# Kernel optimization log

Hardware: AMD Instinct MI355X
Metric: run time of the kernel (lower is better)

The kernel has to match this reference:

```python
import jax, jax.numpy as jnp
import numpy as np

B, S, IN_DIM, LATENT, SYM = 16, 256, 512, 512, 128
NUM_NODES, NUM_CODES, MAX_OPS, MAX_BUS = 4, 512, 4, 32
HALT_EPS, MAX_SEQ = 1e-3, 256


def setup_inputs() -> dict:
    key = jax.random.key(0)
    ks = jax.random.split(key, 10)

    def lin(k, out_d, in_d, pre=()):
        kw, kb = jax.random.split(k)
        lim = 1.0 / np.sqrt(in_d).astype(np.float32)
        w = jax.random.uniform(kw, pre + (out_d, in_d), minval=-lim, maxval=lim, dtype=jnp.float32)
        b = jax.random.uniform(kb, pre + (out_d,), minval=-lim, maxval=lim, dtype=jnp.float32)
        return w, b

    x = jax.random.normal(ks[0], (B, S, IN_DIM), jnp.float32)
    ipw, ipb = lin(ks[1], LATENT, IN_DIM)
    tp = jax.random.normal(ks[2], (1, MAX_SEQ, LATENT), jnp.float32)
    N = (NUM_NODES,)
    sw, sb = lin(ks[3], SYM, LATENT, N)
    qw, qb = lin(ks[4], 1, SYM, N)
    rw, rb = lin(ks[5], LATENT, 2 * LATENT, N)
    c1w, c1b = lin(ks[6], LATENT, LATENT + SYM, N)
    c2w, c2b = lin(ks[7], LATENT, LATENT, N)
    cb = jax.random.normal(ks[8], (NUM_NODES, NUM_CODES, SYM), jnp.float32)
    return {"x": x, "input_proj_w": ipw, "input_proj_b": ipb, "token_prompts": tp,
            "sym_w": sw, "sym_b": sb, "qry_w": qw, "qry_b": qb,
            "read_w": rw, "read_b": rb, "c1_w": c1w, "c1_b": c1b,
            "c2_w": c2w, "c2_b": c2b, "codebook": cb}


def _forward(x, input_proj_w, input_proj_b, token_prompts, sym_w, sym_b, qry_w, qry_b,
             read_w, read_b, c1_w, c1_b, c2_w, c2_b, codebook):
    Bx, Sx, _ = x.shape
    N = Bx * Sx
    # input projection + positional prompts
    out = jnp.einsum('bsi,li->bsl', x, input_proj_w) + input_proj_b + token_prompts[:, :Sx, :]
    prev_out = out
    active = jnp.ones((Bx, Sx), bool)
    token_tags = jnp.zeros((Bx, Sx, SYM), x.dtype)
    # TensorBus rolling buffers ([max_bus, B, S, dim]); with default cfg the roll branch never fires
    sym_buf = jnp.zeros((MAX_BUS, Bx, Sx, SYM), x.dtype)          # slot 0 = zero tags (initial append)
    out_buf = jnp.zeros((MAX_BUS, Bx, Sx, LATENT), x.dtype).at[0].set(out)
    msg_mask = jnp.zeros((MAX_BUS,), bool).at[0].set(True)
    ptr = 1  # static python int: appends are a fixed unrolled schedule (1 + MAX_OPS*NUM_NODES <= MAX_BUS)
    slot_ids = jnp.arange(MAX_BUS)

    for t in range(MAX_OPS):
        # snapshot of active messages for this op step (get_active)
        snap_active = msg_mask & (slot_ids < ptr)                  # [MAX_BUS]
        syms_flat = sym_buf.reshape(MAX_BUS, N, SYM)
        outs_flat = out_buf.reshape(MAX_BUS, N, LATENT)
        keep_all = jnp.ones((MAX_BUS,), bool)
        for n in range(NUM_NODES):
            # relevance of each bus message per token; inactive slots masked out of argmax
            rel = jnp.einsum('tnd,d->tn', syms_flat, qry_w[n, 0]) + qry_b[n, 0]
            rel = jnp.where(snap_active[:, None], rel, jnp.asarray(-1e9, rel.dtype))
            top = jnp.argmax(rel, axis=0)                          # [N] chosen message per token
            chosen = jnp.take_along_axis(outs_flat, top[None, :, None], axis=0)[0]  # [N, LATENT]
            bus_ctx = chosen.reshape(Bx, Sx, LATENT)
            z = jnp.concatenate([out, bus_ctx], axis=-1)
            z_read = jnp.einsum('bsk,lk->bsl', z, read_w[n]) + read_b[n]
            raw_sym = jnp.einsum('bsl,dl->bsd', z_read, sym_w[n]) + sym_b[n]
            # EMA quantizer (eval): nearest codebook entry by euclidean distance
            flat = raw_sym.reshape(-1, SYM)
            cbn = codebook[n]
            d2 = (jnp.sum(flat * flat, axis=-1, keepdims=True)
                  - 2.0 * flat @ cbn.T + jnp.sum(cbn * cbn, axis=-1))
            idx = jnp.argmin(d2, axis=-1)
            quant = cbn[idx].reshape(Bx, Sx, SYM)
            h = jnp.concatenate([z_read, quant], axis=-1)
            hid = jax.nn.relu(jnp.einsum('bsk,lk->bsl', h, c1_w[n]) + c1_b[n])
            node_out = jnp.einsum('bsl,ol->bso', hid, c2_w[n]) + c2_b[n] + out
            # halting / selective update
            delta = jnp.linalg.norm(node_out - prev_out, axis=-1)
            halt = (delta < HALT_EPS) & active
            assigned = active if t > 0 else jnp.ones_like(active)
            upd = assigned & jnp.logical_not(halt)
            out = jnp.where(upd[..., None], node_out, out)
            token_tags = jnp.where(upd[..., None], quant, token_tags)
            # bus.append
            sym_buf = sym_buf.at[ptr].set(quant)
            out_buf = out_buf.at[ptr].set(node_out)
            msg_mask = msg_mask.at[ptr].set(True)
            ptr += 1
            # keep_mask: messages never selected by any token stay alive
            counts = jnp.zeros((MAX_BUS,), jnp.int32).at[top].add(1)
            keep_all = keep_all & (counts == 0)
            active = active & jnp.logical_not(halt)
            prev_out = out
        # mark_consumed: ones over valid slots ANDed with per-node keep masks at snapshot-active
        # slots (inactive/new slots get True -> faithful to the torch init_global_mask quirk)
        msg_mask = (slot_ids < ptr) & keep_all
    return out


def reference(x, input_proj_w, input_proj_b, token_prompts, sym_w, sym_b, qry_w, qry_b,
              read_w, read_b, c1_w, c1_b, c2_w, c2_b, codebook):
    return _forward(x, input_proj_w, input_proj_b, token_prompts, sym_w, sym_b, qry_w, qry_b,
                    read_w, read_b, c1_w, c1_b, c2_w, c2_b, codebook)
```

## Files before the change

kernel.cpp:

```cpp
#include <hip/hip_runtime.h>
#include <math.h>

namespace {

typedef _Float16 f16;
typedef __attribute__((ext_vector_type(8))) _Float16 f16x8;
typedef __attribute__((ext_vector_type(4))) float f32x4;

constexpr int TOK = 4096;
constexpr int DL  = 512;
constexpr int DS  = 128;
constexpr int NC  = 512;
constexpr int NSLOT = 13;

__device__ __forceinline__ float wsum(float v){
  #pragma unroll
  for(int o=32;o>0;o>>=1) v += __shfl_xor(v,o);
  return v;
}

__device__ __forceinline__ void gload16(const void* g, void* l){
  __builtin_amdgcn_global_load_lds(
      (const __attribute__((address_space(1))) unsigned int*)g,
      (__attribute__((address_space(3))) unsigned int*)l, 16, 0, 0);
}

__device__ __forceinline__ int slotb(int row, int g){
  return (((row ^ ((row>>2)&1))<<2) | (g ^ (row&3))) << 4;
}

template<int AMODE,int EPI>
__global__ __launch_bounds__(256,2) void mgemm(
    const f16* __restrict__ A1h, const f16* __restrict__ A1l,
    const f16* __restrict__ A2h, const f16* __restrict__ A2l,
    const f16* __restrict__ Bh, const f16* __restrict__ Bl,
    const float* __restrict__ bias, const float* __restrict__ res,
    float* __restrict__ Cf, f16* __restrict__ Ch, f16* __restrict__ Cl,
    f16* __restrict__ C2h, f16* __restrict__ C2l,
    float* __restrict__ scpv, int* __restrict__ scpi, int* __restrict__ idxg,
    const float* __restrict__ relc, const int* __restrict__ msg,
    int* __restrict__ cons, int pt, int node,
    const float* __restrict__ pq,
    int K, int K0, int ldb)
{
  constexpr int SMB = 16384;
  __shared__ __align__(16) char smem[3*SMB];
  __shared__ int gsel[64];
  __shared__ float redv[4][32];
  __shared__ int   redi[4][32];
  const int tid = threadIdx.x, w = tid>>6, l = tid&63;
  const int m0 = blockIdx.x*64, n0 = blockIdx.y*64;
  const int NK = K>>5, SW = K0>>5;

  if(AMODE==1){
    if(tid<64){
      int m = m0+tid;
      float best = -1e9f; int bs = 0;
      for(int s=0;s<pt;s++){
        float v = msg[s] ? relc[(size_t)((s<<2)+node)*TOK + m] : -1e9f;
        if(v > best){ best=v; bs=s; }
      }
      gsel[tid]=bs;
      cons[bs]=1;
    }
    __syncthreads();
  }
  if(AMODE==3){
    if(tid<64){
      int m = m0+tid;
      float bv = -INFINITY; int bi = 0;
      #pragma unroll
      for(int y=0;y<8;y++){
        float v = scpv[(size_t)y*TOK + m];
        if(v > bv){ bv=v; bi=scpi[(size_t)y*TOK + m]; }
      }
      gsel[tid]=bi;
      idxg[m]=bi;
    }
    __syncthreads();
  }

  const f16* sp[4]; const f16* sp2[4]; int loff[4];
  #pragma unroll
  for(int i=0;i<4;i++){
    int c = 4*w+i;
    int isA = (c<8);
    int plane = isA ? (c>>2) : ((c-8)>>2);
    int cidx  = isA ? (c&3)  : ((c-8)&3);
    loff[i] = (isA?0:8192) + plane*4096 + cidx*1024;
    int s = (cidx<<6) + l;
    int rp = s>>2, row = rp ^ ((rp>>2)&1), g = (s&3) ^ (row&3);
    int g8 = g<<3;
    if(isA){
      int m = m0 + row;
      const f16* p1 = (plane? A1l : A1h) + ((size_t)m<<9) + g8;
      sp[i] = p1;
      if(AMODE==1) sp2[i] = (plane? A2l : A2h) + ((size_t)gsel[row]<<21) + ((size_t)m<<9) + g8;
      else         sp2[i] = p1;
    } else {
      sp[i] = (plane? Bl : Bh) + (size_t)(n0+row)*ldb + g8;
      sp2[i] = sp[i];
    }
  }

  const int wr = w>>1, wc = w&1, q = l>>4, r = l&15;
  int aoff[2], boff[2];
  #pragma unroll
  for(int i=0;i<2;i++) aoff[i] = slotb(32*wr + 16*i + r, q);
  #pragma unroll
  for(int j=0;j<2;j++) boff[j] = 8192 + slotb(32*wc + 16*j + r, q);

  f32x4 acc1[2][2] = {}, acc2[2][2] = {};

  auto advance = [&](int snext){
    #pragma unroll
    for(int i=0;i<4;i++){
      if(AMODE==1 && (4*w+i)<8 && snext==SW) sp[i] = sp2[i];
      else                                    sp[i] += 32;
    }
  };

  #pragma unroll
  for(int i=0;i<4;i++) gload16(sp[i], smem + loff[i]);
  advance(1);
  #pragma unroll
  for(int i=0;i<4;i++) gload16(sp[i], smem + SMB + loff[i]);
  advance(2);
  asm volatile("s_waitcnt vmcnt(4)" ::: "memory");
  __builtin_amdgcn_s_barrier();

  int roff = 0, soff = 2*SMB;
  for(int kt=0; kt<NK; ++kt){
    const char* Lb = smem + roff;
    f16x8 ah[2], al[2], bh[2], bl[2];
    #pragma unroll
    for(int i=0;i<2;i++){
      ah[i] = *(const f16x8*)(Lb + aoff[i]);
      al[i] = *(const f16x8*)(Lb + 4096 + aoff[i]);
    }
    #pragma unroll
    for(int j=0;j<2;j++){
      bh[j] = *(const f16x8*)(Lb + boff[j]);
      bl[j] = *(const f16x8*)(Lb + 4096 + boff[j]);
    }
    if(kt+2 < NK){
      #pragma unroll
      for(int i=0;i<4;i++) gload16(sp[i], smem + soff + loff[i]);
      advance(kt+3);
    }
    #pragma unroll
    for(int i=0;i<2;i++)
      #pragma unroll
      for(int j=0;j<2;j++){
        acc1[i][j] = __builtin_amdgcn_mfma_f32_16x16x32_f16(ah[i], bh[j], acc1[i][j], 0,0,0);
        acc2[i][j] = __builtin_amdgcn_mfma_f32_16x16x32_f16(ah[i], bl[j], acc2[i][j], 0,0,0);
        acc2[i][j] = __builtin_amdgcn_mfma_f32_16x16x32_f16(al[i], bh[j], acc2[i][j], 0,0,0);
      }
    if(kt+2 < NK){
      asm volatile("s_waitcnt vmcnt(4)" ::: "memory");
      __builtin_amdgcn_s_barrier();
    } else if(kt+1 < NK){
      asm volatile("s_waitcnt vmcnt(0)" ::: "memory");
      __builtin_amdgcn_s_barrier();
    }
    roff = (roff==2*SMB)? 0 : roff+SMB;
    soff = (soff==2*SMB)? 0 : soff+SMB;
  }

  if(EPI!=1){
    #pragma unroll
    for(int i=0;i<2;i++)
      #pragma unroll
      for(int j=0;j<2;j++)
        #pragma unroll
        for(int rr=0;rr<4;rr++){
          int lrow = 32*wr + 16*i + 4*q + rr;
          int rowm = m0 + lrow;
          int coln = n0 + 32*wc + 16*j + r;
          size_t o = ((size_t)rowm<<9) + coln;
          float v = acc1[i][j][rr] + acc2[i][j][rr]*(1.0f/2048.0f) + bias[coln];
          if(EPI==5){ v += pq[((size_t)gsel[lrow]<<9) + coln]; v = fmaxf(v, 0.f); }
          if(EPI==3) v += res[o];
          if(EPI==4) v += res[(((size_t)(rowm&255))<<9) + coln];
          if(EPI==3 || EPI==4) Cf[o] = v;
          if(EPI==0 || EPI==4 || EPI==5){
            f16 h = (f16)v;
            Ch[o] = h; Cl[o] = (f16)((v-(float)h)*2048.0f);
          }
          if((EPI==3 || EPI==4) && C2h){
            f16 h = (f16)v;
            C2h[o] = h; C2l[o] = (f16)((v-(float)h)*2048.0f);
          }
        }
  } else {
    #pragma unroll
    for(int i=0;i<2;i++)
      #pragma unroll
      for(int rr=0;rr<4;rr++){
        float v0 = acc1[i][0][rr] + acc2[i][0][rr]*(1.0f/2048.0f) + bias[n0+32*wc+r];
        float v1 = acc1[i][1][rr] + acc2[i][1][rr]*(1.0f/2048.0f) + bias[n0+32*wc+16+r];
        float bv; int bc;
        if(v1 > v0){ bv=v1; bc=n0+32*wc+16+r; } else { bv=v0; bc=n0+32*wc+r; }
        #pragma unroll
        for(int o=1;o<16;o<<=1){
          float ov = __shfl_xor(bv,o); int oi = __shfl_xor(bc,o);
          if(ov>bv || (ov==bv && oi<bc)){ bv=ov; bc=oi; }
        }
        if(r==0){ redv[w][16*i+4*q+rr]=bv; redi[w][16*i+4*q+rr]=bc; }
      }
    __syncthreads();
    if(tid<64){
      int wr2 = tid>>5, li = tid&31;
      float bv = redv[2*wr2][li]; int bc = redi[2*wr2][li];
      float ov = redv[2*wr2+1][li]; int oi = redi[2*wr2+1][li];
      if(ov>bv || (ov==bv && oi<bc)){ bv=ov; bc=oi; }
      scpv[(size_t)blockIdx.y*TOK + m0 + tid] = bv;
      scpi[(size_t)blockIdx.y*TOK + m0 + tid] = bc;
    }
  }
}

__global__ void split_k(const float* __restrict__ src, f16* __restrict__ hi,
                        f16* __restrict__ lo, int n){
  for(int i = blockIdx.x*256 + threadIdx.x; i < n; i += gridDim.x*256){
    float v = src[i];
    f16 h = (f16)v;
    hi[i] = h;
    lo[i] = (f16)((v - (float)h)*2048.0f);
  }
}

struct SplitArg { const float* src; f16* hi; f16* lo; int n; };
struct SplitArgs5 { SplitArg a[5]; };
__global__ void splitm_k(SplitArgs5 A){
  int stride = gridDim.x*256;
  #pragma unroll
  for(int s=0;s<5;s++){
    const float* src = A.a[s].src; f16* hi = A.a[s].hi; f16* lo = A.a[s].lo;
    int n = A.a[s].n;
    for(int i = blockIdx.x*256 + threadIdx.x; i < n; i += stride){
      float v = src[i];
      f16 h = (f16)v;
      hi[i] = h;
      lo[i] = (f16)((v - (float)h)*2048.0f);
    }
  }
}

__global__ __launch_bounds__(256)
void wcomb_k(const float* __restrict__ A, const float* __restrict__ Wall,
             float* __restrict__ C)
{
  constexpr int T=256;
  __shared__ float As[32][68];
  __shared__ float Ws[32][132];
  const int tid = threadIdx.x;
  const int m0 = blockIdx.x*64, n0 = blockIdx.y*128;
  const float* W = Wall + (size_t)(m0>>9)*DS*DL;
  const int ty = tid>>4, tx = tid&15;
  float4 pa[2], pw[4];
  auto loadA = [&](int k0){
    #pragma unroll
    for(int it=0; it<2; ++it){
      int v = tid + T*it; int rr = v>>3, c4 = v&7;
      pa[it] = *(const float4*)(A + (size_t)(m0+rr)*DS + k0 + (c4<<2));
    }
  };
  auto loadW = [&](int k0){
    #pragma unroll
    for(int it=0; it<4; ++it){
      int v = tid + T*it; int rr = v>>5, c4 = v&31;
      pw[it] = *(const float4*)(W + (size_t)(k0+rr)*DL + n0 + (c4<<2));
    }
  };
  float acc[4][8];
  #pragma unroll
  for(int i=0;i<4;i++)
    #pragma unroll
    for(int j=0;j<8;j++) acc[i][j]=0.f;
  loadA(0); loadW(0);
  for(int k0=0; k0<DS; k0+=32){
    __syncthreads();
    #pragma unroll
    for(int it=0; it<2; ++it){
      int v = tid + T*it; int rr=v>>3, c4=v&7;
      As[(c4<<2)+0][rr]=pa[it].x; As[(c4<<2)+1][rr]=pa[it].y;
      As[(c4<<2)+2][rr]=pa[it].z; As[(c4<<2)+3][rr]=pa[it].w;
    }
    #pragma unroll
    for(int it=0; it<4; ++it){
      int v = tid + T*it; int rr=v>>5, c4=v&31;
      *(float4*)&Ws[rr][c4<<2] = pw[it];
    }
    __syncthreads();
    if(k0+32 < DS){ loadA(k0+32); loadW(k0+32); }
    #pragma unroll
    for(int kk=0; kk<32; kk++){
      float4 a4 = *(const float4*)&As[kk][ty<<2];
      float4 b0 = *(const float4*)&Ws[kk][tx<<2];
      float4 b1 = *(const float4*)&Ws[kk][64+(tx<<2)];
      float a[4]={a4.x,a4.y,a4.z,a4.w};
      float b[8]={b0.x,b0.y,b0.z,b0.w,b1.x,b1.y,b1.z,b1.w};
      #pragma unroll
      for(int i=0;i<4;i++)
        #pragma unroll
        for(int j=0;j<8;j++) acc[i][j] = fmaf(a[i], b[j], acc[i][j]);
    }
  }
  #pragma unroll
  for(int i=0;i<4;i++){
    int m = m0 + (ty<<2) + i;
    #pragma unroll
    for(int j=0;j<8;j++){
      int n = n0 + ((j<4)? (tx<<2)+j : 64+(tx<<2)+(j-4));
      C[((size_t)m<<9)+n] = acc[i][j];
    }
  }
}

__global__ __launch_bounds__(256)
void prequant_k(const float* __restrict__ cbp, const float* __restrict__ c1wp,
                float* __restrict__ pq)
{
  constexpr int T=256;
  __shared__ float As[32][68];
  __shared__ float Ws[32][132];
  const int tid = threadIdx.x;
  const int nz = blockIdx.z;
  const int m0 = blockIdx.x*64, n0 = blockIdx.y*128;
  const float* A = cbp  + (size_t)nz*NC*DS;
  const float* W = c1wp + (size_t)nz*DL*640 + 512;
  float* C = pq + (size_t)nz*NC*DL;
  const int ty = tid>>4, tx = tid&15;
  float4 pa[2], pw[4];
  auto loadA = [&](int k0){
    #pragma unroll
    for(int it=0; it<2; ++it){
      int v = tid + T*it; int rr = v>>3, c4 = v&7;
      pa[it] = *(const float4*)(A + (size_t)(m0+rr)*DS + k0 + (c4<<2));
    }
  };
  auto loadW = [&](int k0){
    #pragma unroll
    for(int it=0; it<4; ++it){
      int v = tid + T*it; int rr = v>>3, c4 = v&7;
      pw[it] = *(const float4*)(W + (size_t)(n0+rr)*640 + k0 + (c4<<2));
    }
  };
  float acc[4][8];
  #pragma unroll
  for(int i=0;i<4;i++)
    #pragma unroll
    for(int j=0;j<8;j++) acc[i][j]=0.f;
  loadA(0); loadW(0);
  for(int k0=0; k0<DS; k0+=32){
    __syncthreads();
    #pragma unroll
    for(int it=0; it<2; ++it){
      int v = tid + T*it; int rr=v>>3, c4=v&7;
      As[(c4<<2)+0][rr]=pa[it].x; As[(c4<<2)+1][rr]=pa[it].y;
      As[(c4<<2)+2][rr]=pa[it].z; As[(c4<<2)+3][rr]=pa[it].w;
    }
    #pragma unroll
    for(int it=0; it<4; ++it){
      int v = tid + T*it; int rr=v>>3, c4=v&7;
      Ws[(c4<<2)+0][rr]=pw[it].x; Ws[(c4<<2)+1][rr]=pw[it].y;
      Ws[(c4<<2)+2][rr]=pw[it].z; Ws[(c4<<2)+3][rr]=pw[it].w;
    }
    __syncthreads();
    if(k0+32 < DS){ loadA(k0+32); loadW(k0+32); }
    #pragma unroll
    for(int kk=0; kk<32; kk++){
      float4 a4 = *(const float4*)&As[kk][ty<<2];
      float4 b0 = *(const float4*)&Ws[kk][tx<<2];
      float4 b1 = *(const float4*)&Ws[kk][64+(tx<<2)];
      float a[4]={a4.x,a4.y,a4.z,a4.w};
      float b[8]={b0.x,b0.y,b0.z,b0.w,b1.x,b1.y,b1.z,b1.w};
      #pragma unroll
      for(int i=0;i<4;i++)
        #pragma unroll
        for(int j=0;j<8;j++) acc[i][j] = fmaf(a[i], b[j], acc[i][j]);
    }
  }
  #pragma unroll
  for(int i=0;i<4;i++){
    int m = m0 + (ty<<2) + i;
    #pragma unroll
    for(int j=0;j<8;j++){
      int n = n0 + ((j<4)? (tx<<2)+j : 64+(tx<<2)+(j-4));
      C[((size_t)m<<9)+n] = acc[i][j];
    }
  }
}

__global__ void init_k(int* __restrict__ msg, int* __restrict__ act,
                       float* __restrict__ relc, const float* __restrict__ qb,
                       int* __restrict__ cons){
  int i = blockIdx.x*256 + threadIdx.x;
  if(i < TOK){
    act[i] = 1;
    #pragma unroll
    for(int nn=0;nn<4;nn++) relc[nn*TOK + i] = qb[nn];
  }
  if(i < 32){ msg[i] = (i==0) ? 1 : 0; cons[i] = 0; }
}

__global__ void bias2_k(const float* __restrict__ cb, const float* __restrict__ sb,
                        float* __restrict__ b2){
  int row = blockIdx.x*4 + (threadIdx.x>>6);
  int lane = threadIdx.x&63;
  const float* cv = cb + ((size_t)row<<7);
  const float* sbn = sb + ((row>>9)<<7);
  float c0=cv[lane], c1=cv[lane+64];
  float nrm = c0*c0 + c1*c1;
  float dt  = c0*sbn[lane] + c1*sbn[lane+64];
  nrm = wsum(nrm); dt = wsum(dt);
  if(lane==0) b2[row] = dt - 0.5f*nrm;
}

__global__ void mupdate_k(const float* __restrict__ no_, float* __restrict__ out,
                          f16* __restrict__ outh, f16* __restrict__ outl,
                          float* __restrict__ relc, const int* __restrict__ idx,
                          const float* __restrict__ cbn, const float* __restrict__ qw,
                          const float* __restrict__ qb, int* __restrict__ act,
                          int* __restrict__ cons, int* __restrict__ msg,
                          int t, int ptr, int pe){
  int m = blockIdx.x*4 + (threadIdx.x>>6);
  int lane = threadIdx.x&63;
  const float* nrow = no_ + ((size_t)m<<9);
  float* orow = out + ((size_t)m<<9);
  float nv[8]; float s=0.f;
  #pragma unroll
  for(int rr=0;rr<8;rr++){
    int c = lane + (rr<<6);
    nv[rr]=nrow[c];
    float d = nv[rr]-orow[c]; s += d*d;
  }
  s = wsum(s);
  float delta = sqrtf(s);
  int a = act[m];
  int halt = (delta < 1e-3f) && a;
  int assigned = (t>0) ? a : 1;
  int upd = assigned && !halt;
  if(lane==0) act[m] = a && !halt;
  if(upd){
    #pragma unroll
    for(int rr=0;rr<8;rr++){
      int c = lane + (rr<<6);
      float v = nv[rr];
      orow[c] = v;
      f16 h = (f16)v;
      outh[((size_t)m<<9)+c] = h;
      outl[((size_t)m<<9)+c] = (f16)((v-(float)h)*2048.0f);
    }
  }
  if(ptr >= 0){
    const float* qv = cbn + ((size_t)idx[m]<<7);
    float q0=qv[lane], q1=qv[lane+64];
    #pragma unroll
    for(int nn=0;nn<4;nn++){
      float pr = q0*qw[(nn<<7)+lane] + q1*qw[(nn<<7)+64+lane];
      pr = wsum(pr);
      if(lane==0) relc[(size_t)((ptr<<2)+nn)*TOK + m] = pr + qb[nn];
    }
  }
  if(pe >= 0 && blockIdx.x==0 && threadIdx.x < 32){
    int s2 = threadIdx.x;
    msg[s2] = (s2 < pe) && !cons[s2];
    cons[s2] = 0;
  }
}

}

extern "C" void kernel_launch(void* const* d_in, const int* in_sizes, int n_in,
                              void* d_out, int out_size, void* d_ws, size_t ws_size,
                              hipStream_t stream)
{
  (void)in_sizes; (void)n_in; (void)out_size; (void)ws_size;
  const float* x   = (const float*)d_in[0];
  const float* ipw = (const float*)d_in[1];
  const float* ipb = (const float*)d_in[2];
  const float* tp  = (const float*)d_in[3];
  const float* sw  = (const float*)d_in[4];
  const float* sb  = (const float*)d_in[5];
  const float* qw  = (const float*)d_in[6];
  const float* qb  = (const float*)d_in[7];
  const float* rw  = (const float*)d_in[8];
  const float* rb  = (const float*)d_in[9];
  const float* c1w = (const float*)d_in[10];
  const float* c1b = (const float*)d_in[11];
  const float* c2w = (const float*)d_in[12];
  const float* c2b = (const float*)d_in[13];
  const float* cb  = (const float*)d_in[14];
  float* out = (float*)d_out;

  char* p = (char*)d_ws;
  auto alloc = [&](size_t b)->char*{ char* r=p; p += (b+255)&~(size_t)255; return r; };
  f16* slabh = (f16*)alloc((size_t)NSLOT*TOK*DL*2);
  f16* slabl = (f16*)alloc((size_t)NSLOT*TOK*DL*2);
  f16* outh  = (f16*)alloc((size_t)TOK*DL*2);
  f16* outl  = (f16*)alloc((size_t)TOK*DL*2);
  f16* zh    = (f16*)alloc((size_t)TOK*DL*2);
  f16* zl    = (f16*)alloc((size_t)TOK*DL*2);
  f16* hh    = (f16*)alloc((size_t)TOK*DL*2);
  f16* hl    = (f16*)alloc((size_t)TOK*DL*2);
  float* sn  = (float*)alloc((size_t)TOK*DL*4);
  f16* rwh   = (f16*)alloc((size_t)4*DL*1024*2);
  f16* rwl   = (f16*)alloc((size_t)4*DL*1024*2);
  f16* c1h   = (f16*)alloc((size_t)4*DL*640*2);
  f16* c1l   = (f16*)alloc((size_t)4*DL*640*2);
  f16* c2h   = (f16*)alloc((size_t)4*DL*DL*2);
  f16* c2l   = (f16*)alloc((size_t)4*DL*DL*2);
  f16* wch   = (f16*)alloc((size_t)4*NC*DL*2);
  f16* wcl   = (f16*)alloc((size_t)4*NC*DL*2);
  f16* iph   = (f16*)alloc((size_t)DL*DL*2);
  f16* ipl   = (f16*)alloc((size_t)DL*DL*2);
  f16* cbh   = (f16*)alloc((size_t)4*NC*DS*2);
  f16* cbl   = (f16*)alloc((size_t)4*NC*DS*2);
  float* pq  = (float*)alloc((size_t)4*NC*DL*4);
  float* b2  = (float*)alloc(4*NC*4);
  float* relc= (float*)alloc((size_t)NSLOT*4*TOK*4);
  float* scpv= (float*)alloc((size_t)8*TOK*4);
  int* scpi  = (int*)alloc((size_t)8*TOK*4);
  int* idxb  = (int*)alloc(TOK*4);
  int* act   = (int*)alloc(TOK*4);
  int* msg   = (int*)alloc(256);
  int* cons  = (int*)alloc(256);

  dim3 G(64,8), B(256);

  init_k<<<16,256,0,stream>>>(msg, act, relc, qb, cons);
  bias2_k<<<512,256,0,stream>>>(cb, sb, b2);
  wcomb_k<<<dim3(32,4),B,0,stream>>>(cb, sw, sn);
  prequant_k<<<dim3(8,4,4),B,0,stream>>>(cb, c1w, pq);
  split_k<<<2048,256,0,stream>>>(x, hh, hl, TOK*DL);
  SplitArgs5 sa;
  sa.a[0] = { ipw, iph, ipl, DL*DL };
  sa.a[1] = { rw,  rwh, rwl, 4*DL*1024 };
  sa.a[2] = { c1w, c1h, c1l, 4*DL*640 };
  sa.a[3] = { c2w, c2h, c2l, 4*DL*DL };
  sa.a[4] = { cb,  cbh, cbl, 4*NC*DS };
  splitm_k<<<2048,256,0,stream>>>(sa);
  split_k<<<1024,256,0,stream>>>(sn, wch, wcl, 4*NC*DL);

  mgemm<0,4><<<G,B,0,stream>>>(hh,hl, nullptr,nullptr, iph,ipl,
      ipb, tp, out, outh,outl, slabh,slabl,
      nullptr,nullptr,nullptr, nullptr,nullptr,nullptr, 0,0,
      nullptr, DL, DL, DL);

  int ptr = 1;
  for(int t=0;t<4;t++){
    int pt = 1 + 4*t;
    for(int n=0;n<4;n++){
      mgemm<1,0><<<G,B,0,stream>>>(outh,outl, slabh,slabl,
          rwh+(size_t)n*DL*1024, rwl+(size_t)n*DL*1024, rb+(size_t)n*DL,
          nullptr, nullptr, zh,zl, nullptr,nullptr,
          nullptr,nullptr,nullptr, relc, msg, cons, pt, n,
          nullptr, 1024, 512, 1024);
      mgemm<0,1><<<G,B,0,stream>>>(zh,zl, nullptr,nullptr,
          wch+(size_t)n*NC*DL, wcl+(size_t)n*NC*DL, b2+(size_t)n*NC,
          nullptr, nullptr, nullptr,nullptr, nullptr,nullptr,
          scpv,scpi,nullptr, nullptr,nullptr,nullptr, 0,0,
          nullptr, 512, 512, 512);
      mgemm<3,5><<<G,B,0,stream>>>(zh,zl, nullptr,nullptr,
          c1h+(size_t)n*DL*640, c1l+(size_t)n*DL*640, c1b+(size_t)n*DL,
          nullptr, nullptr, hh,hl, nullptr,nullptr,
          scpv,scpi,idxb, nullptr,nullptr,nullptr, 0,0,
          pq+(size_t)n*NC*DL, 512, 512, 640);
      f16* sph = (t<3) ? slabh + ((size_t)ptr<<21) : nullptr;
      f16* spl = (t<3) ? slabl + ((size_t)ptr<<21) : nullptr;
      mgemm<0,3><<<G,B,0,stream>>>(hh,hl, nullptr,nullptr,
          c2h+(size_t)n*DL*DL, c2l+(size_t)n*DL*DL, c2b+(size_t)n*DL,
          out, sn, nullptr,nullptr, sph,spl,
          nullptr,nullptr,nullptr, nullptr,nullptr,nullptr, 0,0,
          nullptr, 512, 512, 512);
      mupdate_k<<<1024,256,0,stream>>>(sn, out, outh,outl, relc, idxb,
          cb+(size_t)n*NC*DS, qw, qb, act, cons, msg, t,
          (t<3)? ptr : -1, (n==3 && t<3)? (1+4*(t+1)) : -1);
      ptr++;
    }
  }
}
```

Before: 1.280 ms.

## Merge codebook-score and c1 GEMMs into one launch with separate argmax fixup

The codebook scoring GEMM and the c1 latent GEMM now run as a single 16-column-block launch, because both read the same z operand. The argmax over partial scores and the prequantized codebook add plus ReLU move into a new elementwise fixup kernel. The fp32 out buffer is no longer kept per step: the residual and the delta are rebuilt from the hi/lo f16 split, and fp32 out is written only on the final step. This removes one dependent GEMM launch per node and some fp32 traffic, at the cost of an extra intermediate buffer round trip and an extra kernel.

```diff
diff --git a/kernel.cpp b/kernel.cpp
--- a/kernel.cpp
+++ b/kernel.cpp
@@ -37,10 +37,9 @@
     const float* __restrict__ bias, const float* __restrict__ res,
     float* __restrict__ Cf, f16* __restrict__ Ch, f16* __restrict__ Cl,
     f16* __restrict__ C2h, f16* __restrict__ C2l,
-    float* __restrict__ scpv, int* __restrict__ scpi, int* __restrict__ idxg,
+    float* __restrict__ scpv, int* __restrict__ scpi,
     const float* __restrict__ relc, const int* __restrict__ msg,
     int* __restrict__ cons, int pt, int node,
-    const float* __restrict__ pq,
     int K, int K0, int ldb)
 {
   constexpr int SMB = 16384;
@@ -49,7 +48,10 @@
   __shared__ float redv[4][32];
   __shared__ int   redi[4][32];
   const int tid = threadIdx.x, w = tid>>6, l = tid&63;
-  const int m0 = blockIdx.x*64, n0 = blockIdx.y*64;
+  int byy = blockIdx.y;
+  int isS = 1;
+  if(EPI==7 && byy>=8){ isS = 0; byy -= 8; }
+  const int m0 = blockIdx.x*64, n0 = byy*64;
   const int NK = K>>5, SW = K0>>5;
 
   if(AMODE==1){
@@ -65,20 +67,10 @@
     }
     __syncthreads();
   }
-  if(AMODE==3){
-    if(tid<64){
-      int m = m0+tid;
-      float bv = -INFINITY; int bi = 0;
-      #pragma unroll
-      for(int y=0;y<8;y++){
-        float v = scpv[(size_t)y*TOK + m];
-        if(v > bv){ bv=v; bi=scpi[(size_t)y*TOK + m]; }
-      }
-      gsel[tid]=bi;
-      idxg[m]=bi;
-    }
-    __syncthreads();
-  }
+
+  const f16* BhU = (EPI==7 && !isS) ? A2h : Bh;
+  const f16* BlU = (EPI==7 && !isS) ? A2l : Bl;
+  const int ldbU = (EPI==7) ? (isS ? 512 : 640) : ldb;
 
   const f16* sp[4]; const f16* sp2[4]; int loff[4];
   #pragma unroll
@@ -98,7 +90,7 @@
       if(AMODE==1) sp2[i] = (plane? A2l : A2h) + ((size_t)gsel[row]<<21) + ((size_t)m<<9) + g8;
       else         sp2[i] = p1;
     } else {
-      sp[i] = (plane? Bl : Bh) + (size_t)(n0+row)*ldb + g8;
+      sp[i] = (plane? BlU : BhU) + (size_t)(n0+row)*ldbU + g8;
       sp2[i] = sp[i];
     }
   }
@@ -167,32 +159,7 @@
     soff = (soff==2*SMB)? 0 : soff+SMB;
   }
 
-  if(EPI!=1){
-    #pragma unroll
-    for(int i=0;i<2;i++)
-      #pragma unroll
-      for(int j=0;j<2;j++)
-        #pragma unroll
-        for(int rr=0;rr<4;rr++){
-          int lrow = 32*wr + 16*i + 4*q + rr;
-          int rowm = m0 + lrow;
-          int coln = n0 + 32*wc + 16*j + r;
-          size_t o = ((size_t)rowm<<9) + coln;
-          float v = acc1[i][j][rr] + acc2[i][j][rr]*(1.0f/2048.0f) + bias[coln];
-          if(EPI==5){ v += pq[((size_t)gsel[lrow]<<9) + coln]; v = fmaxf(v, 0.f); }
-          if(EPI==3) v += res[o];
-          if(EPI==4) v += res[(((size_t)(rowm&255))<<9) + coln];
-          if(EPI==3 || EPI==4) Cf[o] = v;
-          if(EPI==0 || EPI==4 || EPI==5){
-            f16 h = (f16)v;
-            Ch[o] = h; Cl[o] = (f16)((v-(float)h)*2048.0f);
-          }
-          if((EPI==3 || EPI==4) && C2h){
-            f16 h = (f16)v;
-            C2h[o] = h; C2l[o] = (f16)((v-(float)h)*2048.0f);
-          }
-        }
-  } else {
+  if(EPI==7 ? isS : 0){
     #pragma unroll
     for(int i=0;i<2;i++)
       #pragma unroll
@@ -214,9 +181,57 @@
       float bv = redv[2*wr2][li]; int bc = redi[2*wr2][li];
       float ov = redv[2*wr2+1][li]; int oi = redi[2*wr2+1][li];
       if(ov>bv || (ov==bv && oi<bc)){ bv=ov; bc=oi; }
-      scpv[(size_t)blockIdx.y*TOK + m0 + tid] = bv;
-      scpi[(size_t)blockIdx.y*TOK + m0 + tid] = bc;
-    }
+      scpv[(size_t)byy*TOK + m0 + tid] = bv;
+      scpi[(size_t)byy*TOK + m0 + tid] = bc;
+    }
+  } else {
+    #pragma unroll
+    for(int i=0;i<2;i++)
+      #pragma unroll
+      for(int j=0;j<2;j++)
+        #pragma unroll
+        for(int rr=0;rr<4;rr++){
+          int rowm = m0 + 32*wr + 16*i + 4*q + rr;
+          int coln = n0 + 32*wc + 16*j + r;
+          size_t o = ((size_t)rowm<<9) + coln;
+          float v = acc1[i][j][rr] + acc2[i][j][rr]*(1.0f/2048.0f);
+          if(EPI!=7) v += bias[coln];
+          if(EPI==3) v += (float)A2h[o] + (float)A2l[o]*(1.0f/2048.0f);
+          if(EPI==4) v += res[(((size_t)(rowm&255))<<9) + coln];
+          if(EPI==3 || EPI==4) Cf[o] = v;
+          {
+            f16 h = (f16)v;
+            if(EPI==0 || EPI==4 || EPI==7){ Ch[o] = h; Cl[o] = (f16)((v-(float)h)*2048.0f); }
+            if((EPI==3 || EPI==4) && C2h){ C2h[o] = h; C2l[o] = (f16)((v-(float)h)*2048.0f); }
+          }
+        }
+  }
+}
+
+__global__ __launch_bounds__(256) void fixup_k(
+    const float* __restrict__ scpv, const int* __restrict__ scpi,
+    const f16* __restrict__ hrh, const f16* __restrict__ hrl,
+    const float* __restrict__ pq, const float* __restrict__ c1b,
+    f16* __restrict__ hh, f16* __restrict__ hl, int* __restrict__ idxb)
+{
+  int m = blockIdx.x*4 + (threadIdx.x>>6);
+  int lane = threadIdx.x&63;
+  float bv = -INFINITY; int bi = 0;
+  #pragma unroll
+  for(int y=0;y<8;y++){
+    float v = scpv[(size_t)y*TOK + m];
+    if(v > bv){ bv=v; bi=scpi[(size_t)y*TOK + m]; }
+  }
+  if(lane==0) idxb[m] = bi;
+  const float* pqr = pq + ((size_t)bi<<9);
+  size_t ro = (size_t)m<<9;
+  #pragma unroll
+  for(int rr=0;rr<8;rr++){
+    int c = lane + (rr<<6);
+    float v = (float)hrh[ro+c] + (float)hrl[ro+c]*(1.0f/2048.0f) + pqr[c] + c1b[c];
+    v = fmaxf(v, 0.f);
+    f16 h = (f16)v;
+    hh[ro+c] = h; hl[ro+c] = (f16)((v-(float)h)*2048.0f);
   }
 }
 
@@ -418,23 +433,24 @@
   if(lane==0) b2[row] = dt - 0.5f*nrm;
 }
 
-__global__ void mupdate_k(const float* __restrict__ no_, float* __restrict__ out,
+__global__ void mupdate_k(const float* __restrict__ sn,
                           f16* __restrict__ outh, f16* __restrict__ outl,
-                          float* __restrict__ relc, const int* __restrict__ idx,
+                          float* __restrict__ dout, const int* __restrict__ idx,
                           const float* __restrict__ cbn, const float* __restrict__ qw,
-                          const float* __restrict__ qb, int* __restrict__ act,
-                          int* __restrict__ cons, int* __restrict__ msg,
-                          int t, int ptr, int pe){
+                          const float* __restrict__ qb, float* __restrict__ relc,
+                          int* __restrict__ act, int* __restrict__ cons,
+                          int* __restrict__ msg,
+                          int t, int ptr, int pe, int last){
   int m = blockIdx.x*4 + (threadIdx.x>>6);
   int lane = threadIdx.x&63;
-  const float* nrow = no_ + ((size_t)m<<9);
-  float* orow = out + ((size_t)m<<9);
-  float nv[8]; float s=0.f;
+  size_t ro = (size_t)m<<9;
+  float nv[8], pv[8]; float s = 0.f;
   #pragma unroll
   for(int rr=0;rr<8;rr++){
     int c = lane + (rr<<6);
-    nv[rr]=nrow[c];
-    float d = nv[rr]-orow[c]; s += d*d;
+    nv[rr] = sn[ro+c];
+    pv[rr] = (float)outh[ro+c] + (float)outl[ro+c]*(1.0f/2048.0f);
+    float d = nv[rr]-pv[rr]; s += d*d;
   }
   s = wsum(s);
   float delta = sqrtf(s);
@@ -448,10 +464,16 @@
     for(int rr=0;rr<8;rr++){
       int c = lane + (rr<<6);
       float v = nv[rr];
-      orow[c] = v;
       f16 h = (f16)v;
-      outh[((size_t)m<<9)+c] = h;
-      outl[((size_t)m<<9)+c] = (f16)((v-(float)h)*2048.0f);
+      outh[ro+c] = h;
+      outl[ro+c] = (f16)((v-(float)h)*2048.0f);
+    }
+  }
+  if(last){
+    #pragma unroll
+    for(int rr=0;rr<8;rr++){
+      int c = lane + (rr<<6);
+      dout[ro+c] = upd ? nv[rr] : pv[rr];
     }
   }
   if(ptr >= 0){
@@ -505,6 +527,8 @@
   f16* zl    = (f16*)alloc((size_t)TOK*DL*2);
   f16* hh    = (f16*)alloc((size_t)TOK*DL*2);
   f16* hl    = (f16*)alloc((size_t)TOK*DL*2);
+  f16* hrh   = (f16*)alloc((size_t)TOK*DL*2);
+  f16* hrl   = (f16*)alloc((size_t)TOK*DL*2);
   float* sn  = (float*)alloc((size_t)TOK*DL*4);
   f16* rwh   = (f16*)alloc((size_t)4*DL*1024*2);
   f16* rwl   = (f16*)alloc((size_t)4*DL*1024*2);
@@ -516,8 +540,6 @@
   f16* wcl   = (f16*)alloc((size_t)4*NC*DL*2);
   f16* iph   = (f16*)alloc((size_t)DL*DL*2);
   f16* ipl   = (f16*)alloc((size_t)DL*DL*2);
-  f16* cbh   = (f16*)alloc((size_t)4*NC*DS*2);
-  f16* cbl   = (f16*)alloc((size_t)4*NC*DS*2);
   float* pq  = (float*)alloc((size_t)4*NC*DL*4);
   float* b2  = (float*)alloc(4*NC*4);
   float* relc= (float*)alloc((size_t)NSLOT*4*TOK*4);
@@ -528,7 +550,7 @@
   int* msg   = (int*)alloc(256);
   int* cons  = (int*)alloc(256);
 
-  dim3 G(64,8), B(256);
+  dim3 G(64,8), Gm(64,16), B(256);
 
   init_k<<<16,256,0,stream>>>(msg, act, relc, qb, cons);
   bias2_k<<<512,256,0,stream>>>(cb, sb, b2);
@@ -540,14 +562,13 @@
   sa.a[1] = { rw,  rwh, rwl, 4*DL*1024 };
   sa.a[2] = { c1w, c1h, c1l, 4*DL*640 };
   sa.a[3] = { c2w, c2h, c2l, 4*DL*DL };
-  sa.a[4] = { cb,  cbh, cbl, 4*NC*DS };
+  sa.a[4] = { x,   hrh, hrl, 1 };
   splitm_k<<<2048,256,0,stream>>>(sa);
   split_k<<<1024,256,0,stream>>>(sn, wch, wcl, 4*NC*DL);
 
   mgemm<0,4><<<G,B,0,stream>>>(hh,hl, nullptr,nullptr, iph,ipl,
       ipb, tp, out, outh,outl, slabh,slabl,
-      nullptr,nullptr,nullptr, nullptr,nullptr,nullptr, 0,0,
-      nullptr, DL, DL, DL);
+      nullptr,nullptr, nullptr,nullptr,nullptr, 0,0, DL, DL, DL);
 
   int ptr = 1;
   for(int t=0;t<4;t++){
@@ -556,28 +577,24 @@
       mgemm<1,0><<<G,B,0,stream>>>(outh,outl, slabh,slabl,
           rwh+(size_t)n*DL*1024, rwl+(size_t)n*DL*1024, rb+(size_t)n*DL,
           nullptr, nullptr, zh,zl, nullptr,nullptr,
-          nullptr,nullptr,nullptr, relc, msg, cons, pt, n,
-          nullptr, 1024, 512, 1024);
-      mgemm<0,1><<<G,B,0,stream>>>(zh,zl, nullptr,nullptr,
+          nullptr,nullptr, relc, msg, cons, pt, n, 1024, 512, 1024);
+      mgemm<0,7><<<Gm,B,0,stream>>>(zh,zl,
+          c1h+(size_t)n*DL*640, c1l+(size_t)n*DL*640,
           wch+(size_t)n*NC*DL, wcl+(size_t)n*NC*DL, b2+(size_t)n*NC,
-          nullptr, nullptr, nullptr,nullptr, nullptr,nullptr,
-          scpv,scpi,nullptr, nullptr,nullptr,nullptr, 0,0,
-          nullptr, 512, 512, 512);
-      mgemm<3,5><<<G,B,0,stream>>>(zh,zl, nullptr,nullptr,
-          c1h+(size_t)n*DL*640, c1l+(size_t)n*DL*640, c1b+(size_t)n*DL,
-          nullptr, nullptr, hh,hl, nullptr,nullptr,
-          scpv,scpi,idxb, nullptr,nullptr,nullptr, 0,0,
-          pq+(size_t)n*NC*DL, 512, 512, 640);
+          nullptr, nullptr, hrh,hrl, nullptr,nullptr,
+          scpv,scpi, nullptr,nullptr,nullptr, 0,0, 512, 512, 512);
+      fixup_k<<<1024,256,0,stream>>>(scpv, scpi, hrh, hrl,
+          pq+(size_t)n*NC*DL, c1b+(size_t)n*DL, hh, hl, idxb);
       f16* sph = (t<3) ? slabh + ((size_t)ptr<<21) : nullptr;
       f16* spl = (t<3) ? slabl + ((size_t)ptr<<21) : nullptr;
-      mgemm<0,3><<<G,B,0,stream>>>(hh,hl, nullptr,nullptr,
+      mgemm<0,3><<<G,B,0,stream>>>(hh,hl, outh,outl,
           c2h+(size_t)n*DL*DL, c2l+(size_t)n*DL*DL, c2b+(size_t)n*DL,
-          out, sn, nullptr,nullptr, sph,spl,
-          nullptr,nullptr,nullptr, nullptr,nullptr,nullptr, 0,0,
-          nullptr, 512, 512, 512);
-      mupdate_k<<<1024,256,0,stream>>>(sn, out, outh,outl, relc, idxb,
-          cb+(size_t)n*NC*DS, qw, qb, act, cons, msg, t,
-          (t<3)? ptr : -1, (n==3 && t<3)? (1+4*(t+1)) : -1);
+          nullptr, sn, nullptr,nullptr, sph,spl,
+          nullptr,nullptr, nullptr,nullptr,nullptr, 0,0, 512, 512, 512);
+      mupdate_k<<<1024,256,0,stream>>>(sn, outh,outl, out, idxb,
+          cb+(size_t)n*NC*DS, qw, qb, relc, act, cons, msg, t,
+          (t<3)? ptr : -1, (n==3 && t<3)? (1+4*(t+1)) : -1,
+          (t==3 && n==3)? 1 : 0);
       ptr++;
     }
   }
```

Measured after the change: 1.313 ms. 1.03x slower.
